# Performance work log

Hardware: AMD Instinct MI355X
Metric: run time of the kernel (lower is better)

The kernel has to match this reference:

```python
import jax, jax.numpy as jnp
import numpy as np

K = 32            # number of stocks to select (init kwarg k)
TEMP = 1.0        # initial_temperature, no annealing applied
EPS = 1e-10
MASK_SUB = 10000.0


def setup_inputs() -> dict:
    key = jax.random.key(0)
    k1, k2 = jax.random.split(key)
    scores = jax.random.normal(k1, (4096, 8192), dtype=jnp.float32)
    u = jax.random.uniform(k2, (4096, 8192), dtype=jnp.float32)
    return {"scores": scores, "u": u}


def reference(scores, u):
    # gumbel noise exactly as torch: -log(-log(rand + eps) + eps)
    gumbel = -jnp.log(-jnp.log(u + EPS) + EPS)
    perturbed = (scores + gumbel) / TEMP

    # iterative soft top-k: k rounds of softmax + suppress selected mass
    def step(carry, _):
        soft_mask, remaining = carry
        s = jax.nn.softmax(remaining, axis=-1)
        return (soft_mask + s, remaining - s * MASK_SUB), None

    (soft_mask, _), _ = jax.lax.scan(
        step, (jnp.zeros_like(scores), perturbed), None, length=K)

    # hard top-k mask from raw scores
    _, idx = jax.lax.top_k(scores, K)                      # (B, K)
    B = scores.shape[0]
    hard_mask = jnp.zeros_like(scores).at[
        jnp.arange(B)[:, None], idx].set(1.0)

    # straight-through: forward == hard_mask, backward through soft_mask
    return hard_mask - jax.lax.stop_gradient(soft_mask) + soft_mask
```

## Files before the change

### kernel.cpp

```cpp
#include <hip/hip_runtime.h>


constexpr int ROWS = 4096;
constexpr int COLS = 8192;
constexpr int TPB  = 256;
constexpr int VPT  = COLS / TPB / 4;
constexpr int KSEL = 32;
constexpr int CAP  = 1024;

__device__ __forceinline__ unsigned f2key(float f) {
    unsigned b = __float_as_uint(f);
    return (b & 0x80000000u) ? ~b : (b | 0x80000000u);
}

__global__ __launch_bounds__(TPB, 4) void topk_mask_kernel(
        const float* __restrict__ scores, float* __restrict__ out) {
    const int tid = threadIdx.x;
    const size_t base = (size_t)blockIdx.x * COLS;
    const float4* __restrict__ src = reinterpret_cast<const float4*>(scores + base);
    float4*       __restrict__ dst = reinterpret_cast<float4*>(out + base);

    __shared__ __align__(16) unsigned       ckey[CAP];
    __shared__ __align__(16) unsigned short cidx[CAP];
    __shared__ unsigned bitmap[COLS / 32];
    __shared__ unsigned cnt;

    float4 vv[VPT];
#pragma unroll
    for (int j = 0; j < VPT; ++j) vv[j] = src[tid + j * TPB];

    reinterpret_cast<uint4*>(ckey)[tid] = make_uint4(0, 0, 0, 0);
    bitmap[tid] = 0;
    if (tid == 0) cnt = 0;
    __syncthreads();

    unsigned C;
    for (int attempt = 0; ; ++attempt) {
        const float tval = (attempt == 0) ? 2.0f
                         : (attempt == 1) ? 0.0f
                         : (attempt == 2) ? -2.0f : -3.4e38f;
        const unsigned tkey = f2key(tval);
#pragma unroll
        for (int j = 0; j < VPT; ++j) {
            const float f[4] = {vv[j].x, vv[j].y, vv[j].z, vv[j].w};
#pragma unroll
            for (int c = 0; c < 4; ++c) {
                const unsigned k = f2key(f[c]);
                if (k > tkey) {
                    const unsigned p = atomicAdd(&cnt, 1u);
                    if (p < CAP) {
                        ckey[p] = k;
                        cidx[p] = (unsigned short)(4 * (tid + j * TPB) + c);
                    }
                }
            }
        }
        __syncthreads();
        C = cnt;
        if (C >= (unsigned)KSEL || attempt >= 3) break;
        __syncthreads();
        if (tid == 0) cnt = 0;
        reinterpret_cast<uint4*>(ckey)[tid] = make_uint4(0, 0, 0, 0);
        __syncthreads();
    }
    if (C > (unsigned)CAP) C = CAP;

    {
        const unsigned C4 = (C + 3) >> 2;
        const uint4*   ck4 = reinterpret_cast<const uint4*>(ckey);
        const ushort4* ci4 = reinterpret_cast<const ushort4*>(cidx);
        for (unsigned q = tid; q < C; q += TPB) {
            const unsigned kq = ckey[q];
            const unsigned iq = cidx[q];
            unsigned r = 0;
            for (unsigned p = 0; p < C4; ++p) {
                const uint4   kk = ck4[p];
                const ushort4 ii = ci4[p];
                r += (kk.x > kq) + (kk.y > kq) + (kk.z > kq) + (kk.w > kq);
                r += (kk.x == kq && ii.x < iq);
                r += (kk.y == kq && ii.y < iq);
                r += (kk.z == kq && ii.z < iq);
                r += (kk.w == kq && ii.w < iq);
            }
            if (r < (unsigned)KSEL)
                atomicOr(&bitmap[iq >> 5], 1u << (iq & 31u));
        }
    }
    __syncthreads();

#pragma unroll
    for (int j = 0; j < VPT; ++j) {
        const unsigned w  = bitmap[(tid >> 3) + 32 * j];
        const unsigned sh = 4u * (tid & 7u);
        float4 o;
        o.x = ((w >> (sh + 0)) & 1u) ? 1.0f : 0.0f;
        o.y = ((w >> (sh + 1)) & 1u) ? 1.0f : 0.0f;
        o.z = ((w >> (sh + 2)) & 1u) ? 1.0f : 0.0f;
        o.w = ((w >> (sh + 3)) & 1u) ? 1.0f : 0.0f;
        dst[tid + j * TPB] = o;
    }
}

extern "C" void kernel_launch(void* const* d_in, const int* in_sizes, int n_in,
                              void* d_out, int out_size, void* d_ws, size_t ws_size,
                              hipStream_t stream) {
    const float* scores = (const float*)d_in[0];
    float* out = (float*)d_out;
    topk_mask_kernel<<<dim3(ROWS), dim3(TPB), 0, stream>>>(scores, out);
}
```

Before: 284.8 us.

## Process one row per wavefront with ballot-compaction and packed key-index sort

Each 64-lane wavefront now owns a whole row instead of each block owning one, so the per-row synchronisation becomes wave-local and needs no __syncthreads. Candidate collection uses __ballot/popcount prefix compaction instead of shared-memory atomics, with higher thresholds so fewer candidates are kept. Keys and indices are packed into 64-bit values, which reduces the rank comparison to one compare per element. The scores are re-read from global memory on each threshold attempt instead of being held in registers, and ties are broken toward the lower index through the packed encoding.

```diff
diff --git a/kernel.cpp b/kernel.cpp
--- a/kernel.cpp
+++ b/kernel.cpp
@@ -1,12 +1,14 @@
 #include <hip/hip_runtime.h>
 
 
-constexpr int ROWS = 4096;
-constexpr int COLS = 8192;
-constexpr int TPB  = 256;
-constexpr int VPT  = COLS / TPB / 4;
-constexpr int KSEL = 32;
-constexpr int CAP  = 1024;
+constexpr int ROWS  = 4096;
+constexpr int COLS  = 8192;
+constexpr int TPB   = 256;
+constexpr int WAVES = TPB / 64;
+constexpr int CPL   = COLS / 64 / 4;
+constexpr int KSEL  = 32;
+constexpr int CAPW  = 256;
+constexpr int BMW   = COLS / 32;
 
 __device__ __forceinline__ unsigned f2key(float f) {
     unsigned b = __float_as_uint(f);
@@ -15,89 +17,85 @@
 
 __global__ __launch_bounds__(TPB, 4) void topk_mask_kernel(
         const float* __restrict__ scores, float* __restrict__ out) {
-    const int tid = threadIdx.x;
-    const size_t base = (size_t)blockIdx.x * COLS;
+    const int tid  = threadIdx.x;
+    const int wv   = tid >> 6;
+    const int lane = tid & 63;
+    const int row  = blockIdx.x * WAVES + wv;
+    const size_t base = (size_t)row * COLS;
     const float4* __restrict__ src = reinterpret_cast<const float4*>(scores + base);
     float4*       __restrict__ dst = reinterpret_cast<float4*>(out + base);
 
-    __shared__ __align__(16) unsigned       ckey[CAP];
-    __shared__ __align__(16) unsigned short cidx[CAP];
-    __shared__ unsigned bitmap[COLS / 32];
-    __shared__ unsigned cnt;
+    __shared__ __align__(16) unsigned long long skey[WAVES][CAPW];
+    __shared__ __align__(16) unsigned           bmsh[WAVES][BMW];
+    unsigned long long* sk  = skey[wv];
+    unsigned*           bmw = bmsh[wv];
 
-    float4 vv[VPT];
+    reinterpret_cast<uint4*>(bmw)[lane] = make_uint4(0u, 0u, 0u, 0u);
+
+    const unsigned long long ltm = (1ull << lane) - 1ull;
+
+    unsigned cnt = 0;
+    for (int attempt = 0; ; ++attempt) {
+        const float T = (attempt == 0) ? 2.3f
+                      : (attempt == 1) ? 1.9f
+                      : (attempt == 2) ? 0.0f : -3.0e38f;
+        cnt = 0;
 #pragma unroll
-    for (int j = 0; j < VPT; ++j) vv[j] = src[tid + j * TPB];
+        for (int s = 0; s < CAPW / 64; ++s) sk[lane + 64 * s] = 0ull;
 
-    reinterpret_cast<uint4*>(ckey)[tid] = make_uint4(0, 0, 0, 0);
-    bitmap[tid] = 0;
-    if (tid == 0) cnt = 0;
-    __syncthreads();
-
-    unsigned C;
-    for (int attempt = 0; ; ++attempt) {
-        const float tval = (attempt == 0) ? 2.0f
-                         : (attempt == 1) ? 0.0f
-                         : (attempt == 2) ? -2.0f : -3.4e38f;
-        const unsigned tkey = f2key(tval);
-#pragma unroll
-        for (int j = 0; j < VPT; ++j) {
-            const float f[4] = {vv[j].x, vv[j].y, vv[j].z, vv[j].w};
+#pragma unroll 8
+        for (int t = 0; t < CPL; ++t) {
+            const float4 v = src[lane + 64 * t];
+            const float f[4] = {v.x, v.y, v.z, v.w};
 #pragma unroll
             for (int c = 0; c < 4; ++c) {
-                const unsigned k = f2key(f[c]);
-                if (k > tkey) {
-                    const unsigned p = atomicAdd(&cnt, 1u);
-                    if (p < CAP) {
-                        ckey[p] = k;
-                        cidx[p] = (unsigned short)(4 * (tid + j * TPB) + c);
+                const bool pr = f[c] > T;
+                const unsigned long long m = __ballot(pr);
+                if (m) {
+                    if (pr) {
+                        const unsigned pos = cnt + (unsigned)__popcll(m & ltm);
+                        if (pos < CAPW) {
+                            const unsigned idx = 4u * (unsigned)(lane + 64 * t) + c;
+                            sk[pos] = ((unsigned long long)f2key(f[c]) << 13)
+                                      | (unsigned long long)(8191u - idx);
+                        }
                     }
+                    cnt += (unsigned)__popcll(m);
                 }
             }
         }
-        __syncthreads();
-        C = cnt;
-        if (C >= (unsigned)KSEL || attempt >= 3) break;
-        __syncthreads();
-        if (tid == 0) cnt = 0;
-        reinterpret_cast<uint4*>(ckey)[tid] = make_uint4(0, 0, 0, 0);
-        __syncthreads();
+        if (cnt >= (unsigned)KSEL || attempt >= 3) break;
     }
-    if (C > (unsigned)CAP) C = CAP;
+    const unsigned C = cnt < (unsigned)CAPW ? cnt : (unsigned)CAPW;
 
     {
-        const unsigned C4 = (C + 3) >> 2;
-        const uint4*   ck4 = reinterpret_cast<const uint4*>(ckey);
-        const ushort4* ci4 = reinterpret_cast<const ushort4*>(cidx);
-        for (unsigned q = tid; q < C; q += TPB) {
-            const unsigned kq = ckey[q];
-            const unsigned iq = cidx[q];
+        const ulonglong2* sk2 = reinterpret_cast<const ulonglong2*>(sk);
+        const unsigned NP = (C + 1u) >> 1;
+        const unsigned NS = (C + 63u) >> 6;
+        for (unsigned s = 0; s < NS; ++s) {
+            const unsigned long long kq = sk[lane + 64u * s];
             unsigned r = 0;
-            for (unsigned p = 0; p < C4; ++p) {
-                const uint4   kk = ck4[p];
-                const ushort4 ii = ci4[p];
-                r += (kk.x > kq) + (kk.y > kq) + (kk.z > kq) + (kk.w > kq);
-                r += (kk.x == kq && ii.x < iq);
-                r += (kk.y == kq && ii.y < iq);
-                r += (kk.z == kq && ii.z < iq);
-                r += (kk.w == kq && ii.w < iq);
+            for (unsigned p = 0; p < NP; ++p) {
+                const ulonglong2 kk = sk2[p];
+                r += (kk.x > kq) + (kk.y > kq);
             }
-            if (r < (unsigned)KSEL)
-                atomicOr(&bitmap[iq >> 5], 1u << (iq & 31u));
+            if (r < (unsigned)KSEL && kq != 0ull) {
+                const unsigned idx = 8191u - (unsigned)(kq & 0x1FFFull);
+                atomicOr(&bmw[idx >> 5], 1u << (idx & 31u));
+            }
         }
     }
-    __syncthreads();
 
-#pragma unroll
-    for (int j = 0; j < VPT; ++j) {
-        const unsigned w  = bitmap[(tid >> 3) + 32 * j];
-        const unsigned sh = 4u * (tid & 7u);
+    const unsigned sh = 4u * (unsigned)(lane & 7);
+#pragma unroll 8
+    for (int t = 0; t < CPL; ++t) {
+        const unsigned w = bmw[(lane >> 3) + 8 * t];
         float4 o;
         o.x = ((w >> (sh + 0)) & 1u) ? 1.0f : 0.0f;
         o.y = ((w >> (sh + 1)) & 1u) ? 1.0f : 0.0f;
         o.z = ((w >> (sh + 2)) & 1u) ? 1.0f : 0.0f;
         o.w = ((w >> (sh + 3)) & 1u) ? 1.0f : 0.0f;
-        dst[tid + j * TPB] = o;
+        dst[lane + 64 * t] = o;
     }
 }
 
@@ -106,5 +104,5 @@
                               hipStream_t stream) {
     const float* scores = (const float*)d_in[0];
     float* out = (float*)d_out;
-    topk_mask_kernel<<<dim3(ROWS), dim3(TPB), 0, stream>>>(scores, out);
+    topk_mask_kernel<<<dim3(ROWS / WAVES), dim3(TPB), 0, stream>>>(scores, out);
 }
```

After: 283.3 us. About the same (-0.5%).
